# Kernel tuning notes

Hardware: AMD Instinct MI355X
Metric: run time of the kernel (lower is better)

## Reference

```python
import jax, jax.numpy as jnp
import numpy as np

B, S, H, NH, FF = 8, 512, 1024, 16, 4096
DK = H // NH


def _ln(x, g, b):
    m = x.mean(-1, keepdims=True)
    v = ((x - m) ** 2).mean(-1, keepdims=True)
    return (x - m) / jnp.sqrt(v + 1e-5) * g + b


def _fwd(x, predicate_pos, attn_bias, attention_mask, atom_graph, variable_graph,
         ln1_g, ln1_b, wq, bq, wk, bk, wv, bv, wo, bo,
         pq_w, pq_b, pk_w, pk_b, pv_w, pv_b, ln2_g, ln2_b, w1, b1, w2, b2):
    b_, s_, h_ = x.shape
    y = _ln(x, ln1_g, ln1_b)
    # ---- self attention (manual MHA with additive bias + mask) ----
    scale = DK ** -0.5
    q = (y @ wq + bq).reshape(b_, s_, NH, DK) * scale
    k = (y @ wk + bk).reshape(b_, s_, NH, DK)
    v = (y @ wv + bv).reshape(b_, s_, NH, DK)
    scores = jnp.einsum('bihd,bjhd->bhij', q, k)
    scores = scores + attn_bias[:, None, :, :] + attention_mask[:, None, :, :]
    att = jax.nn.softmax(scores, axis=-1)
    y_self = jnp.einsum('bhij,bjhd->bihd', att, v).reshape(b_, s_, h_) @ wo + bo
    # ---- path attention (single-head with graph biases) ----
    pscale = h_ ** -0.5
    pq = (y @ pq_w + pq_b) * pscale
    pk = y @ pk_w + pk_b
    pv = y @ pv_w + pv_b
    patt = jnp.einsum('bid,bjd->bij', pq, pk) + atom_graph + variable_graph
    patt = jax.nn.softmax(patt, axis=-1)
    xp = jnp.einsum('bij,bjd->bid', patt, pv)  # [B,S,H]
    # vectorized gather-mean over predicate positions (replaces per-sample loop)
    prev = jnp.concatenate([xp[:, :1], xp[:, :-1]], axis=1)   # xp[i-1]
    nxt = jnp.concatenate([xp[:, 1:], xp[:, -1:]], axis=1)    # xp[i+1]
    a0 = xp[:, 0:2].mean(axis=1, keepdims=True)               # i == 0
    a1 = xp[:, 0:3].mean(axis=1, keepdims=True)               # i == 1
    a2 = (xp + nxt) / 2.0                                     # pos[i-2] == 1
    a3 = (prev + xp + nxt) / 3.0                              # else
    i_arr = jnp.arange(s_)
    pos = (predicate_pos == 1)
    pos_m2 = jnp.pad(pos[:, :-2], ((0, 0), (2, 0)))           # pos[i-2], False for i<2
    atom = jnp.where(pos_m2[..., None], a2, a3)
    atom = jnp.where((i_arr == 1)[None, :, None], a1, atom)
    atom = jnp.where((i_arr == 0)[None, :, None], a0, atom)
    w = pos.astype(xp.dtype)
    path = (atom * w[..., None]).sum(1) / w.sum(1, keepdims=True)  # [B,H]
    y_path = jnp.broadcast_to(path[:, None, :], (b_, s_, h_))
    # ---- combine + residual + FFN ----
    x = x + (y_self + y_path) / 2.0
    y2 = _ln(x, ln2_g, ln2_b)
    hmid = jax.nn.gelu(y2 @ w1 + b1, approximate=False)
    return x + (hmid @ w2 + b2)


def setup_inputs() -> dict:
    key = jax.random.key(0)
    ks = jax.random.split(key, 16)
    def w(k, shape):
        return 0.02 * jax.random.normal(k, shape, dtype=jnp.float32)
    pp = jax.random.randint(ks[0], (B, S), 0, 2, dtype=jnp.int32)
    pp = pp.at[:, 2].set(1).at[:, -1].set(0)  # >=1 predicate; no predicate at last node
    return {
        'x': jax.random.normal(ks[1], (B, S, H), dtype=jnp.float32),
        'predicate_pos': pp,
        'variable_tags': jnp.zeros((B, S), dtype=jnp.int32),
        'attn_bias': 0.1 * jax.random.normal(ks[2], (B, S, S), dtype=jnp.float32),
        'attention_mask': jnp.zeros((B, S, S), dtype=jnp.float32),
        'atom_graph': 0.1 * jax.random.normal(ks[3], (B, S, S), dtype=jnp.float32),
        'variable_graph': 0.1 * jax.random.normal(ks[4], (B, S, S), dtype=jnp.float32),
        'ln1_g': jnp.ones((H,), jnp.float32), 'ln1_b': jnp.zeros((H,), jnp.float32),
        'wq': w(ks[5], (H, H)), 'bq': jnp.zeros((H,), jnp.float32),
        'wk': w(ks[6], (H, H)), 'bk': jnp.zeros((H,), jnp.float32),
        'wv': w(ks[7], (H, H)), 'bv': jnp.zeros((H,), jnp.float32),
        'wo': w(ks[8], (H, H)), 'bo': jnp.zeros((H,), jnp.float32),
        'pq_w': w(ks[9], (H, H)), 'pq_b': jnp.zeros((H,), jnp.float32),
        'pk_w': w(ks[10], (H, H)), 'pk_b': jnp.zeros((H,), jnp.float32),
        'pv_w': w(ks[11], (H, H)), 'pv_b': jnp.zeros((H,), jnp.float32),
        'ln2_g': jnp.ones((H,), jnp.float32), 'ln2_b': jnp.zeros((H,), jnp.float32),
        'w1': w(ks[12], (H, FF)), 'b1': jnp.zeros((FF,), jnp.float32),
        'w2': w(ks[13], (FF, H)), 'b2': jnp.zeros((H,), jnp.float32),
    }


def reference(x, predicate_pos, variable_tags, attn_bias, attention_mask, atom_graph, variable_graph,
              ln1_g, ln1_b, wq, bq, wk, bk, wv, bv, wo, bo,
              pq_w, pq_b, pk_w, pk_b, pv_w, pv_b, ln2_g, ln2_b, w1, b1, w2, b2):
    # variable_tags is unused in the original forward as well
    return _fwd(x, predicate_pos, attn_bias, attention_mask, atom_graph, variable_graph,
                ln1_g, ln1_b, wq, bq, wk, bk, wv, bv, wo, bo,
                pq_w, pq_b, pk_w, pk_b, pv_w, pv_b, ln2_g, ln2_b, w1, b1, w2, b2)
```

## Files before the change

kernel.cpp:

```cpp
#include <hip/hip_runtime.h>
#include <hip/hip_bf16.h>
#include <math.h>


typedef __bf16 bf16x8 __attribute__((ext_vector_type(8)));
typedef float f32x4 __attribute__((ext_vector_type(4)));

__device__ __forceinline__ void async_copy16(void* lds, const void* g) {
  __builtin_amdgcn_global_load_lds(
      (__attribute__((address_space(1))) void*)(void*)g,
      (__attribute__((address_space(3))) void*)lds, 16, 0, 0);
}

#define SB0 __builtin_amdgcn_sched_barrier(0)
#define BARRIER __builtin_amdgcn_s_barrier()

__global__ __launch_bounds__(256) void ln_rows_bf16(
    const float* __restrict__ X, const float* __restrict__ G,
    const float* __restrict__ Bt, __hip_bfloat16* __restrict__ O) {
  long row = blockIdx.x;
  int t = threadIdx.x;
  const float4 xv = ((const float4*)(X + row * 1024))[t];
  float s = xv.x + xv.y + xv.z + xv.w;
  float q = xv.x * xv.x + xv.y * xv.y + xv.z * xv.z + xv.w * xv.w;
#pragma unroll
  for (int o = 32; o; o >>= 1) {
    s += __shfl_xor(s, o);
    q += __shfl_xor(q, o);
  }
  __shared__ float rs[4], rq[4];
  int wid = t >> 6;
  if ((t & 63) == 0) { rs[wid] = s; rq[wid] = q; }
  __syncthreads();
  s = rs[0] + rs[1] + rs[2] + rs[3];
  q = rq[0] + rq[1] + rq[2] + rq[3];
  float mean = s * (1.f / 1024.f);
  float var = q * (1.f / 1024.f) - mean * mean;
  float rstd = rsqrtf(var + 1e-5f);
  const float4 gv = ((const float4*)G)[t];
  const float4 bv = ((const float4*)Bt)[t];
  __hip_bfloat16* o = O + row * 1024 + t * 4;
  o[0] = __float2bfloat16((xv.x - mean) * rstd * gv.x + bv.x);
  o[1] = __float2bfloat16((xv.y - mean) * rstd * gv.y + bv.y);
  o[2] = __float2bfloat16((xv.z - mean) * rstd * gv.z + bv.z);
  o[3] = __float2bfloat16((xv.w - mean) * rstd * gv.w + bv.w);
}

struct TC7 {
  const float* in[7];
  __hip_bfloat16* out[7];
  float scale[7];
};
__global__ __launch_bounds__(256) void tconv7(TC7 p) {
  __shared__ float t[32][33];
  int j = blockIdx.z;
  const float* in = p.in[j];
  __hip_bfloat16* out = p.out[j];
  float sc = p.scale[j];
  int c0 = blockIdx.x * 32, r0 = blockIdx.y * 32;
  int tid = threadIdx.x;
  int lr = tid >> 3, lc = (tid & 7) * 4;
  const float4 v = *(const float4*)&in[(long)(r0 + lr) * 1024 + c0 + lc];
  t[lr][lc] = v.x; t[lr][lc + 1] = v.y; t[lr][lc + 2] = v.z; t[lr][lc + 3] = v.w;
  __syncthreads();
  int oc = tid >> 3, orr = (tid & 7) * 4;
  __hip_bfloat16* o = &out[(long)(c0 + oc) * 1024 + r0 + orr];
  o[0] = __float2bfloat16(t[orr][oc] * sc);
  o[1] = __float2bfloat16(t[orr + 1][oc] * sc);
  o[2] = __float2bfloat16(t[orr + 2][oc] * sc);
  o[3] = __float2bfloat16(t[orr + 3][oc] * sc);
}

__global__ __launch_bounds__(256) void tconv_f32_bf16(
    const float* __restrict__ in, __hip_bfloat16* __restrict__ out, int R,
    int C) {
  __shared__ float t[32][33];
  int c0 = blockIdx.x * 32, r0 = blockIdx.y * 32;
  int tid = threadIdx.x;
  int lr = tid >> 3, lc = (tid & 7) * 4;
  const float4 v = *(const float4*)&in[(long)(r0 + lr) * C + c0 + lc];
  t[lr][lc] = v.x; t[lr][lc + 1] = v.y; t[lr][lc + 2] = v.z; t[lr][lc + 3] = v.w;
  __syncthreads();
  int oc = tid >> 3, orr = (tid & 7) * 4;
  __hip_bfloat16* o = &out[(long)(c0 + oc) * R + r0 + orr];
  o[0] = __float2bfloat16(t[orr][oc]);
  o[1] = __float2bfloat16(t[orr + 1][oc]);
  o[2] = __float2bfloat16(t[orr + 2][oc]);
  o[3] = __float2bfloat16(t[orr + 3][oc]);
}

__global__ __launch_bounds__(256) void tconv_bf16(
    const __hip_bfloat16* __restrict__ in, __hip_bfloat16* __restrict__ out,
    int R, int C, int ldin, long sIn) {
  __shared__ __hip_bfloat16 t[32][34];
  int bz = blockIdx.z;
  long ibase = (long)bz * sIn;
  long obase = (long)bz * R * C;
  int c0 = blockIdx.x * 32, r0 = blockIdx.y * 32;
  int tid = threadIdx.x;
  int lr = tid >> 3, lc = (tid & 7) * 4;
  const __hip_bfloat16* ip = &in[ibase + (long)(r0 + lr) * ldin + c0 + lc];
  t[lr][lc] = ip[0]; t[lr][lc + 1] = ip[1]; t[lr][lc + 2] = ip[2]; t[lr][lc + 3] = ip[3];
  __syncthreads();
  int oc = tid >> 3, orr = (tid & 7) * 4;
  __hip_bfloat16* o = &out[obase + (long)(c0 + oc) * R + r0 + orr];
  o[0] = t[orr][oc];
  o[1] = t[orr + 1][oc];
  o[2] = t[orr + 2][oc];
  o[3] = t[orr + 3][oc];
}

struct BC6 {
  const float* b[6];
  float scale[6];
};
__global__ __launch_bounds__(256) void bias_concat(BC6 p, float* __restrict__ o) {
  int idx = blockIdx.x * 256 + threadIdx.x;
  int j = idx >> 10, e = idx & 1023;
  o[idx] = p.b[j][e] * p.scale[j];
}

template <int BN>
__global__ __launch_bounds__(512, 2) void gemm256(
    const __hip_bfloat16* __restrict__ A, const __hip_bfloat16* __restrict__ Bt,
    const float* __restrict__ bias, void* __restrict__ C, int K, int lda,
    int ldb, int ldc, int act, int obf, long sC) {
  constexpr int NR = BN / 64;
  constexpr int ABYTES = 256 * 128;
  constexpr int BBYTES = BN * 128;
  constexpr int BUF = ABYTES + BBYTES;
  __shared__ char lds[2 * BUF];

  int bx, by;
  {
    int wg = blockIdx.y * gridDim.x + blockIdx.x;
    int gx = gridDim.x, gy = gridDim.y;
    if ((gx & 3) == 0 && (gy & 1) == 0) {
      int cw = gx >> 2, ch = gy >> 1;
      int xcd = wg & 7, idx = wg >> 3;
      bx = (xcd & 3) * cw + idx % cw;
      by = (xcd >> 2) * ch + idx / cw;
    } else {
      bx = blockIdx.x;
      by = blockIdx.y;
    }
  }
  const int m0 = by * 256, n0 = bx * BN;
  const int z = blockIdx.z;
  const long kbase = (long)z * K * 2;

  const int tid = threadIdx.x;
  const int lane = tid & 63, wid = tid >> 6;
  const int wm = wid >> 2, wn = wid & 3;
  const int ll = lane & 15, lh = lane >> 4;

  const char* Ag = (const char*)A;
  const char* Bg = (const char*)Bt;
  const int srow = tid >> 3;
  const int scb = (((tid & 7) ^ (srow & 7)) << 4);
  const int sld = (tid & 7) << 4;

  auto stageA = [&](char* base, long kb) {
#pragma unroll
    for (int l = 0; l < 4; ++l) {
      int row = l * 64 + srow;
      async_copy16(base + row * 128 + sld,
                   Ag + ((long)(m0 + row) * lda) * 2 + kb + scb);
    }
  };
  auto stageB = [&](char* base, long kb) {
#pragma unroll
    for (int l = 0; l < BN / 64; ++l) {
      int row = l * 64 + srow;
      async_copy16(base + ABYTES + row * 128 + sld,
                   Bg + ((long)(n0 + row) * ldb) * 2 + kb + scb);
    }
  };

  const int rx = ll & 7;
  const int ck[2] = {((0 + lh) ^ rx) << 4, ((4 + lh) ^ rx) << 4};

  f32x4 acc[8][NR];
#pragma unroll
  for (int m = 0; m < 8; ++m)
#pragma unroll
    for (int n = 0; n < NR; ++n) acc[m][n] = (f32x4){0.f, 0.f, 0.f, 0.f};

  const int nt = K >> 6;
  stageA(lds, kbase);
  stageB(lds, kbase);

  for (int t = 0; t < nt; ++t) {
    const int bt = t & 1;
    const char* Ab = lds + bt * BUF;
    const char* Bb = Ab + ABYTES;
    char* nb = lds + (bt ^ 1) * BUF;
    const bool pre = (t + 1 < nt);

    SB0; BARRIER; SB0;
    if (pre) {
      const long kb = kbase + (long)(t + 1) * 128;
      stageA(nb, kb);
      stageB(nb, kb);
      if constexpr (BN == 256)
        asm volatile("s_waitcnt vmcnt(8)" ::: "memory");
      else if constexpr (BN == 192)
        asm volatile("s_waitcnt vmcnt(7)" ::: "memory");
      else
        asm volatile("s_waitcnt vmcnt(6)" ::: "memory");
    } else {
      asm volatile("s_waitcnt vmcnt(0)" ::: "memory");
    }
    SB0; BARRIER; SB0;

#pragma unroll
    for (int ks = 0; ks < 2; ++ks) {
      bf16x8 bf[NR];
#pragma unroll
      for (int n = 0; n < NR; ++n)
        bf[n] = *(const bf16x8*)(Bb + (wn * (BN / 4) + n * 16 + ll) * 128 +
                                 ck[ks]);
      bf16x8 af[4];
#pragma unroll
      for (int m = 0; m < 4; ++m)
        af[m] = *(const bf16x8*)(Ab + (wm * 128 + m * 16 + ll) * 128 + ck[ks]);
      __builtin_amdgcn_s_setprio(1);
#pragma unroll
      for (int m = 0; m < 4; ++m)
#pragma unroll
        for (int n = 0; n < NR; ++n)
          acc[m][n] = __builtin_amdgcn_mfma_f32_16x16x32_bf16(af[m], bf[n],
                                                              acc[m][n], 0, 0, 0);
      __builtin_amdgcn_s_setprio(0);
#pragma unroll
      for (int m = 0; m < 4; ++m)
        af[m] = *(const bf16x8*)(Ab + (wm * 128 + (m + 4) * 16 + ll) * 128 +
                                 ck[ks]);
      __builtin_amdgcn_s_setprio(1);
#pragma unroll
      for (int m = 0; m < 4; ++m)
#pragma unroll
        for (int n = 0; n < NR; ++n)
          acc[m + 4][n] = __builtin_amdgcn_mfma_f32_16x16x32_bf16(
              af[m], bf[n], acc[m + 4][n], 0, 0, 0);
      __builtin_amdgcn_s_setprio(0);
    }
  }

#pragma unroll
  for (int m = 0; m < 8; ++m) {
    int row = m0 + wm * 128 + m * 16 + lh * 4;
#pragma unroll
    for (int n = 0; n < NR; ++n) {
      int col = n0 + wn * (BN / 4) + n * 16 + ll;
      float bs = bias ? bias[col] : 0.f;
#pragma unroll
      for (int r = 0; r < 4; ++r) {
        float v = acc[m][n][r] + bs;
        if (act) v = v * 0.5f * (1.f + erff(v * 0.70710678118f));
        long cidx = (long)z * sC + (long)(row + r) * ldc + col;
        if (obf)
          ((__hip_bfloat16*)C)[cidx] = __float2bfloat16(v);
        else
          ((float*)C)[cidx] = v;
      }
    }
  }
}

__global__ __launch_bounds__(256) void ffn2_reduce(
    const float* __restrict__ P, const float* __restrict__ X2,
    const float* __restrict__ b2, float* __restrict__ OUT) {
  int i = blockIdx.x * 256 + threadIdx.x;
  const long SP = 4194304;
  float4 a = ((const float4*)P)[i];
  float4 b = ((const float4*)(P + SP))[i];
  float4 c = ((const float4*)(P + 2 * SP))[i];
  float4 d = ((const float4*)(P + 3 * SP))[i];
  float4 xr = ((const float4*)X2)[i];
  const float4 bb = *(const float4*)(b2 + ((i & 255) * 4));
  float4 o;
  o.x = a.x + b.x + c.x + d.x + xr.x + bb.x;
  o.y = a.y + b.y + c.y + d.y + xr.y + bb.y;
  o.z = a.z + b.z + c.z + d.z + xr.z + bb.z;
  o.w = a.w + b.w + c.w + d.w + xr.w + bb.w;
  ((float4*)OUT)[i] = o;
}

__global__ __launch_bounds__(256) void gemm_bf16_nt(
    const __hip_bfloat16* __restrict__ A, const __hip_bfloat16* __restrict__ Bt,
    const float* __restrict__ bias, const float* __restrict__ E1,
    const float* __restrict__ E2, void* __restrict__ C, int K, int lda,
    int ldb, int ldc, long sA, long sB, long sC, long sE, float alpha, int act,
    int obf, int pbc) {
  __shared__ unsigned short AsU[128 * 32];
  __shared__ unsigned short BsU[128 * 32];
  const int tid = threadIdx.x;
  const int lane = tid & 63, wave = tid >> 6;
  const int wr = wave >> 1, wc = wave & 1;

  int nwg = gridDim.x * gridDim.y;
  int wg = blockIdx.y * gridDim.x + blockIdx.x;
  int bx = blockIdx.x, by = blockIdx.y;
  if ((nwg & 7) == 0) {
    int cpx = nwg >> 3;
    int sw = (wg & 7) * cpx + (wg >> 3);
    bx = sw % gridDim.x;
    by = sw / gridDim.x;
  }
  const int m0 = by * 128, n0 = bx * 128;
  const int bz = blockIdx.z;
  const char* Ab = (const char*)(A + (long)bz * sA);
  const char* Bb = (const char*)(Bt + (long)bz * sB);

  f32x4 acc[4][4];
#pragma unroll
  for (int m = 0; m < 4; ++m)
#pragma unroll
    for (int n = 0; n < 4; ++n) acc[m][n] = (f32x4){0.f, 0.f, 0.f, 0.f};

  const int srow = tid >> 2;
  const int scol = (tid & 3) * 16;
  const int wbase = (tid >> 6) * 1024;

  for (int k0 = 0; k0 < K; k0 += 32) {
#pragma unroll
    for (int i = 0; i < 2; ++i) {
      async_copy16((char*)AsU + i * 4096 + wbase,
                   Ab + ((long)(m0 + i * 64 + srow) * lda + k0) * 2 + scol);
      async_copy16((char*)BsU + i * 4096 + wbase,
                   Bb + ((long)(n0 + i * 64 + srow) * ldb + k0) * 2 + scol);
    }
    __syncthreads();

    const int koff = (lane >> 4) * 8;
    bf16x8 a[4], b[4];
#pragma unroll
    for (int m = 0; m < 4; ++m)
      a[m] = *(const bf16x8*)&AsU[(wr * 64 + m * 16 + (lane & 15)) * 32 + koff];
#pragma unroll
    for (int n = 0; n < 4; ++n)
      b[n] = *(const bf16x8*)&BsU[(wc * 64 + n * 16 + (lane & 15)) * 32 + koff];
#pragma unroll
    for (int m = 0; m < 4; ++m)
#pragma unroll
      for (int n = 0; n < 4; ++n)
        acc[m][n] = __builtin_amdgcn_mfma_f32_16x16x32_bf16(a[m], b[n],
                                                            acc[m][n], 0, 0, 0);
    __syncthreads();
  }

#pragma unroll
  for (int m = 0; m < 4; ++m) {
    int row = m0 + wr * 64 + m * 16 + (lane >> 4) * 4;
#pragma unroll
    for (int n = 0; n < 4; ++n) {
      int col = n0 + wc * 64 + n * 16 + (lane & 15);
      float bs = bias ? bias[col] : 0.f;
#pragma unroll
      for (int r = 0; r < 4; ++r) {
        float v = (acc[m][n][r] + bs) * alpha;
        if (pbc) {
          v = E1[(long)(row + r) * ldc + col] +
              0.5f * (v + E2[(long)((row + r) >> 9) * 1024 + col]);
        } else {
          long eidx = (long)bz * sE + (long)(row + r) * ldc + col;
          if (E1) v += E1[eidx];
          if (E2) v += E2[eidx];
        }
        if (act) v = v * 0.5f * (1.f + erff(v * 0.70710678118f));
        long cidx = (long)bz * sC + (long)(row + r) * ldc + col;
        if (obf)
          ((__hip_bfloat16*)C)[cidx] = __float2bfloat16(v);
        else
          ((float*)C)[cidx] = v;
      }
    }
  }
}

__global__ __launch_bounds__(256) void attn_mfma(
    const __hip_bfloat16* __restrict__ Q, const __hip_bfloat16* __restrict__ K,
    const __hip_bfloat16* __restrict__ VT, const float* __restrict__ BiasP,
    const float* __restrict__ MaskP, __hip_bfloat16* __restrict__ O,
    int ldqk) {
  __shared__ __hip_bfloat16 P[32][520];
  __shared__ float red[2][32][4];
  const int it = blockIdx.x, h = blockIdx.y, b = blockIdx.z;
  const int i0 = it * 32;
  const int tid = threadIdx.x;
  const int lane = tid & 63, w = tid >> 6;
  const int lh = lane >> 4, ll = lane & 15;

  const long qkb = (long)b * 512 * ldqk + h * 64;

  bf16x8 a[2][2];
#pragma unroll
  for (int m = 0; m < 2; ++m)
#pragma unroll
    for (int ks = 0; ks < 2; ++ks)
      a[m][ks] = *(const bf16x8*)&Q[qkb + (long)(i0 + m * 16 + ll) * ldqk +
                                    ks * 32 + lh * 8];

  f32x4 acc[2][8];
#pragma unroll
  for (int m = 0; m < 2; ++m)
#pragma unroll
    for (int n = 0; n < 8; ++n) acc[m][n] = (f32x4){0.f, 0.f, 0.f, 0.f};

#pragma unroll
  for (int n = 0; n < 8; ++n) {
    const __hip_bfloat16* kp =
        &K[qkb + (long)(w * 128 + n * 16 + ll) * ldqk + lh * 8];
    bf16x8 b0 = *(const bf16x8*)&kp[0];
    bf16x8 b1 = *(const bf16x8*)&kp[32];
#pragma unroll
    for (int m = 0; m < 2; ++m) {
      acc[m][n] =
          __builtin_amdgcn_mfma_f32_16x16x32_bf16(a[m][0], b0, acc[m][n], 0, 0, 0);
      acc[m][n] =
          __builtin_amdgcn_mfma_f32_16x16x32_bf16(a[m][1], b1, acc[m][n], 0, 0, 0);
    }
  }

  const long bmo = ((long)b * 512 + i0) * 512 + w * 128;
#pragma unroll
  for (int m = 0; m < 2; ++m)
#pragma unroll
    for (int r = 0; r < 4; ++r) {
      int row = m * 16 + lh * 4 + r;
#pragma unroll
      for (int n = 0; n < 8; ++n) {
        long gi = bmo + (long)row * 512 + n * 16 + ll;
        acc[m][n][r] += BiasP[gi] + MaskP[gi];
      }
    }

  float rmax[2][4];
#pragma unroll
  for (int m = 0; m < 2; ++m)
#pragma unroll
    for (int r = 0; r < 4; ++r) {
      float v = acc[m][0][r];
#pragma unroll
      for (int n = 1; n < 8; ++n) v = fmaxf(v, acc[m][n][r]);
#pragma unroll
      for (int o = 1; o < 16; o <<= 1) v = fmaxf(v, __shfl_xor(v, o));
      rmax[m][r] = v;
    }
  if (ll == 0) {
#pragma unroll
    for (int m = 0; m < 2; ++m)
#pragma unroll
      for (int r = 0; r < 4; ++r) red[0][m * 16 + lh * 4 + r][w] = rmax[m][r];
  }
  __syncthreads();
#pragma unroll
  for (int m = 0; m < 2; ++m)
#pragma unroll
    for (int r = 0; r < 4; ++r) {
      const float* p = red[0][m * 16 + lh * 4 + r];
      rmax[m][r] = fmaxf(fmaxf(p[0], p[1]), fmaxf(p[2], p[3]));
    }
  float rsum[2][4];
#pragma unroll
  for (int m = 0; m < 2; ++m)
#pragma unroll
    for (int r = 0; r < 4; ++r) {
      float s = 0.f;
#pragma unroll
      for (int n = 0; n < 8; ++n) {
        float e = __expf(acc[m][n][r] - rmax[m][r]);
        acc[m][n][r] = e;
        s += e;
      }
#pragma unroll
      for (int o = 1; o < 16; o <<= 1) s += __shfl_xor(s, o);
      rsum[m][r] = s;
    }
  if (ll == 0) {
#pragma unroll
    for (int m = 0; m < 2; ++m)
#pragma unroll
      for (int r = 0; r < 4; ++r) red[1][m * 16 + lh * 4 + r][w] = rsum[m][r];
  }
  __syncthreads();
#pragma unroll
  for (int m = 0; m < 2; ++m)
#pragma unroll
    for (int r = 0; r < 4; ++r) {
      const float* p = red[1][m * 16 + lh * 4 + r];
      float inv = 1.f / (p[0] + p[1] + p[2] + p[3]);
      int row = m * 16 + lh * 4 + r;
#pragma unroll
      for (int n = 0; n < 8; ++n)
        P[row][w * 128 + n * 16 + ll] = __float2bfloat16(acc[m][n][r] * inv);
    }
  __syncthreads();

  const long vtb = ((long)b * 1024 + h * 64) * 512;
  const long ob = (long)b * 512 * 1024 + h * 64;
  const int mw = (w >> 1) * 16, nw = (w & 1) * 32;
  f32x4 oacc[2];
  oacc[0] = (f32x4){0.f, 0.f, 0.f, 0.f};
  oacc[1] = (f32x4){0.f, 0.f, 0.f, 0.f};
#pragma unroll
  for (int ks = 0; ks < 16; ++ks) {
    int k0 = ks * 32;
    bf16x8 pa = *(const bf16x8*)&P[mw + ll][k0 + lh * 8];
#pragma unroll
    for (int nf = 0; nf < 2; ++nf) {
      bf16x8 vb = *(const bf16x8*)&VT[vtb + (long)(nw + nf * 16 + ll) * 512 +
                                      k0 + lh * 8];
      oacc[nf] =
          __builtin_amdgcn_mfma_f32_16x16x32_bf16(pa, vb, oacc[nf], 0, 0, 0);
    }
  }
#pragma unroll
  for (int nf = 0; nf < 2; ++nf)
#pragma unroll
    for (int r = 0; r < 4; ++r)
      O[ob + (long)(i0 + mw + lh * 4 + r) * 1024 + nw + nf * 16 + ll] =
          __float2bfloat16(oacc[nf][r]);
}

__global__ __launch_bounds__(256) void softmax_rows(
    const float* __restrict__ P, __hip_bfloat16* __restrict__ Ob) {
  const float* row = P + (long)blockIdx.x * 512;
  __hip_bfloat16* orow = Ob + (long)blockIdx.x * 512;
  int t = threadIdx.x;
  float v0 = row[t], v1 = row[t + 256];
  float m = fmaxf(v0, v1);
#pragma unroll
  for (int o = 32; o; o >>= 1) m = fmaxf(m, __shfl_xor(m, o));
  __shared__ float red[8];
  int wid = t >> 6, lane = t & 63;
  if (!lane) red[wid] = m;
  __syncthreads();
  m = fmaxf(fmaxf(red[0], red[1]), fmaxf(red[2], red[3]));
  float e0 = __expf(v0 - m), e1 = __expf(v1 - m);
  float s = e0 + e1;
#pragma unroll
  for (int o = 32; o; o >>= 1) s += __shfl_xor(s, o);
  if (!lane) red[4 + wid] = s;
  __syncthreads();
  s = red[4] + red[5] + red[6] + red[7];
  float inv = 1.f / s;
  orow[t] = __float2bfloat16(e0 * inv);
  orow[t + 256] = __float2bfloat16(e1 * inv);
}

__global__ __launch_bounds__(256) void path_partial(
    const float* __restrict__ xp, const int* __restrict__ pp,
    float* __restrict__ PP, float* __restrict__ WS) {
  int b = blockIdx.x, hc = blockIdx.y, ic = blockIdx.z;
  int h = hc * 256 + threadIdx.x;
  const int* ppb = pp + b * 512;
  const float* xb = xp + (long)b * 512 * 1024;
  int iA = ic * 64, iB = iA + 64;
  float acc = 0.f;
  for (int i = iA; i < iB; ++i) {
    if (ppb[i] != 1) continue;
    float cur = xb[(long)i * 1024 + h];
    float a;
    if (i == 0) {
      a = 0.5f * (cur + xb[1024 + h]);
    } else if (i == 1) {
      a = (xb[h] + cur + xb[2 * 1024 + h]) * (1.f / 3.f);
    } else {
      int inx = (i + 1 < 512) ? i + 1 : 511;
      float nx = xb[(long)inx * 1024 + h];
      if (ppb[i - 2] == 1) {
        a = 0.5f * (cur + nx);
      } else {
        a = (xb[(long)(i - 1) * 1024 + h] + cur + nx) * (1.f / 3.f);
      }
    }
    acc += a;
  }
  PP[((long)b * 8 + ic) * 1024 + h] = acc;
  if (hc == 0 && threadIdx.x == 0) {
    float c = 0.f;
    for (int i = iA; i < iB; ++i) c += (ppb[i] == 1) ? 1.f : 0.f;
    WS[b * 8 + ic] = c;
  }
}

__global__ __launch_bounds__(256) void path_finalize(
    const float* __restrict__ PP, const float* __restrict__ WS,
    float* __restrict__ PATH) {
  int b = blockIdx.x;
  int h = blockIdx.y * 256 + threadIdx.x;
  float s = 0.f, w = 0.f;
#pragma unroll
  for (int ic = 0; ic < 8; ++ic) {
    s += PP[((long)b * 8 + ic) * 1024 + h];
    w += WS[b * 8 + ic];
  }
  PATH[b * 1024 + h] = s / w;
}

extern "C" void kernel_launch(void* const* d_in, const int* in_sizes, int n_in,
                              void* d_out, int out_size, void* d_ws,
                              size_t ws_size, hipStream_t stream) {
  const float* x = (const float*)d_in[0];
  const int* pp = (const int*)d_in[1];
  const float* abias = (const float*)d_in[3];
  const float* amask = (const float*)d_in[4];
  const float* agraph = (const float*)d_in[5];
  const float* vgraph = (const float*)d_in[6];
  const float* ln1g = (const float*)d_in[7];
  const float* ln1b = (const float*)d_in[8];
  const float* wq = (const float*)d_in[9];
  const float* bq = (const float*)d_in[10];
  const float* wk = (const float*)d_in[11];
  const float* bk = (const float*)d_in[12];
  const float* wv = (const float*)d_in[13];
  const float* bv = (const float*)d_in[14];
  const float* wo = (const float*)d_in[15];
  const float* bo = (const float*)d_in[16];
  const float* pqw = (const float*)d_in[17];
  const float* pqb = (const float*)d_in[18];
  const float* pkw = (const float*)d_in[19];
  const float* pkb = (const float*)d_in[20];
  const float* pvw = (const float*)d_in[21];
  const float* pvb = (const float*)d_in[22];
  const float* ln2g = (const float*)d_in[23];
  const float* ln2b = (const float*)d_in[24];
  const float* w1 = (const float*)d_in[25];
  const float* b1 = (const float*)d_in[26];
  const float* w2 = (const float*)d_in[27];
  const float* b2 = (const float*)d_in[28];

  char* wsb = (char*)d_ws;
  auto Ybf = (__hip_bfloat16*)(wsb);
  auto QKV = (__hip_bfloat16*)(wsb + (8l << 20));
  auto VTb = (__hip_bfloat16*)(wsb + (56l << 20));
  auto PVT = (__hip_bfloat16*)(wsb + (64l << 20));
  auto ATTb = (__hip_bfloat16*)(wsb + (72l << 20));
  auto PATTb = (__hip_bfloat16*)(wsb + (88l << 20));
  auto PATTf = (float*)(wsb + (92l << 20));
  auto XP = (float*)(wsb + (92l << 20));
  auto WALL = (__hip_bfloat16*)(wsb + (108l << 20));
  auto WOT = (__hip_bfloat16*)(wsb + (120l << 20));
  auto W1T = (__hip_bfloat16*)(wsb + (122l << 20));
  auto bias6 = (float*)(wsb + (130l << 20));
  auto PPart = (float*)(wsb + (131l << 20));
  auto WSp = (float*)(wsb + (132l << 20));
  auto PATH = (float*)(wsb + (133l << 20));
  auto X2 = (float*)(wsb + (24l << 20));
  auto HMID = (__hip_bfloat16*)(wsb + (40l << 20));
  auto W2T = ATTb;
  auto PART = (float*)(wsb + (92l << 20));
  __hip_bfloat16* Y2b = Ybf;
  float* OUT = (float*)d_out;

  const float qscale = 0.125f;
  const float pscale = 0.03125f;
  const long S2 = 512l * 512;
  const long SQ = 512l * 6144;

  __hip_bfloat16* Qp = QKV;
  __hip_bfloat16* Kp = QKV + 1024;
  __hip_bfloat16* Vp = QKV + 2048;
  __hip_bfloat16* PQp = QKV + 3072;
  __hip_bfloat16* PKp = QKV + 4096;
  __hip_bfloat16* PVp = QKV + 5120;

  TC7 tp;
  tp.in[0] = wq;  tp.out[0] = WALL;                 tp.scale[0] = qscale;
  tp.in[1] = wk;  tp.out[1] = WALL + 1024 * 1024;   tp.scale[1] = 1.f;
  tp.in[2] = wv;  tp.out[2] = WALL + 2048 * 1024;   tp.scale[2] = 1.f;
  tp.in[3] = pqw; tp.out[3] = WALL + 3072 * 1024;   tp.scale[3] = pscale;
  tp.in[4] = pkw; tp.out[4] = WALL + 4096 * 1024;   tp.scale[4] = 1.f;
  tp.in[5] = pvw; tp.out[5] = WALL + 5120 * 1024;   tp.scale[5] = 1.f;
  tp.in[6] = wo;  tp.out[6] = WOT;                  tp.scale[6] = 1.f;
  tconv7<<<dim3(32, 32, 7), 256, 0, stream>>>(tp);
  tconv_f32_bf16<<<dim3(128, 32), 256, 0, stream>>>(w1, W1T, 1024, 4096);

  BC6 bp;
  bp.b[0] = bq;  bp.scale[0] = qscale;
  bp.b[1] = bk;  bp.scale[1] = 1.f;
  bp.b[2] = bv;  bp.scale[2] = 1.f;
  bp.b[3] = pqb; bp.scale[3] = pscale;
  bp.b[4] = pkb; bp.scale[4] = 1.f;
  bp.b[5] = pvb; bp.scale[5] = 1.f;
  bias_concat<<<24, 256, 0, stream>>>(bp, bias6);

  ln_rows_bf16<<<4096, 256, 0, stream>>>(x, ln1g, ln1b, Ybf);

  gemm256<192><<<dim3(32, 16, 1), 512, 0, stream>>>(
      Ybf, WALL, bias6, QKV, 1024, 1024, 1024, 6144, 0, 1, 0);

  tconv_bf16<<<dim3(32, 16, 8), 256, 0, stream>>>(Vp, VTb, 512, 1024, 6144, SQ);
  tconv_bf16<<<dim3(32, 16, 8), 256, 0, stream>>>(PVp, PVT, 512, 1024, 6144, SQ);

  gemm_bf16_nt<<<dim3(4, 4, 8), 256, 0, stream>>>(
      PQp, PKp, nullptr, agraph, vgraph, PATTf, 1024, 6144, 6144, 512, SQ, SQ,
      S2, S2, 1.f, 0, 0, 0);
  softmax_rows<<<4096, 256, 0, stream>>>(PATTf, PATTb);

  attn_mfma<<<dim3(16, 16, 8), 256, 0, stream>>>(Qp, Kp, VTb, abias, amask,
                                                 ATTb, 6144);

  gemm_bf16_nt<<<dim3(8, 4, 8), 256, 0, stream>>>(
      PATTb, PVT, nullptr, nullptr, nullptr, XP, 512, 512, 512, 1024, S2,
      512l * 1024, 512l * 1024, 0, 1.f, 0, 0, 0);

  path_partial<<<dim3(8, 4, 8), 256, 0, stream>>>(XP, pp, PPart, WSp);
  path_finalize<<<dim3(8, 4), 256, 0, stream>>>(PPart, WSp, PATH);

  gemm_bf16_nt<<<dim3(8, 32, 1), 256, 0, stream>>>(
      ATTb, WOT, bo, x, PATH, X2, 1024, 1024, 1024, 1024, 0, 0, 0, 0, 1.f, 0,
      0, 1);

  tconv_f32_bf16<<<dim3(32, 128), 256, 0, stream>>>(w2, W2T, 4096, 1024);

  ln_rows_bf16<<<4096, 256, 0, stream>>>(X2, ln2g, ln2b, Y2b);

  gemm256<256><<<dim3(16, 16, 1), 512, 0, stream>>>(
      Y2b, W1T, b1, HMID, 1024, 1024, 1024, 4096, 1, 1, 0);

  gemm256<256><<<dim3(4, 16, 4), 512, 0, stream>>>(
      HMID, W2T, nullptr, PART, 1024, 4096, 4096, 1024, 0, 0, 4194304);

  ffn2_reduce<<<4096, 256, 0, stream>>>(PART, X2, b2, OUT);
}
```

Baseline: 470.4 us.

## Double-buffer LDS in NT GEMM and split-K the path score GEMM

The generic NT GEMM now keeps two LDS buffers. It issues async global-to-LDS copies for the next K tile while MFMAs run on the current one, and raises wave priority around the MFMA block. It also gains a K-split parameter. The path-attention score GEMM uses it with two splits to double the block count on an undersubscribed grid, and the softmax kernel sums the two fp32 partials before normalising. The costs are double the LDS footprint, which may reduce occupancy, an extra 8 MB partial buffer in the workspace that must not overlap other data, and extra read traffic in the softmax.

```diff
diff --git a/kernel.cpp b/kernel.cpp
--- a/kernel.cpp
+++ b/kernel.cpp
@@ -292,9 +292,9 @@
     const float* __restrict__ bias, const float* __restrict__ E1,
     const float* __restrict__ E2, void* __restrict__ C, int K, int lda,
     int ldb, int ldc, long sA, long sB, long sC, long sE, float alpha, int act,
-    int obf, int pbc) {
-  __shared__ unsigned short AsU[128 * 32];
-  __shared__ unsigned short BsU[128 * 32];
+    int obf, int pbc, int ksplit, long sSplit) {
+  __shared__ unsigned short AsU[2][128 * 32];
+  __shared__ unsigned short BsU[2][128 * 32];
   const int tid = threadIdx.x;
   const int lane = tid & 63, wave = tid >> 6;
   const int wr = wave >> 1, wc = wave & 1;
@@ -309,7 +309,10 @@
     by = sw / gridDim.x;
   }
   const int m0 = by * 128, n0 = bx * 128;
-  const int bz = blockIdx.z;
+  const int bz = blockIdx.z / ksplit;
+  const int sk = blockIdx.z % ksplit;
+  if (sk != 0) { bias = nullptr; E1 = nullptr; E2 = nullptr; }
+  const int kcol0 = sk * K;
   const char* Ab = (const char*)(A + (long)bz * sA);
   const char* Bb = (const char*)(Bt + (long)bz * sB);
 
@@ -323,31 +326,49 @@
   const int scol = (tid & 3) * 16;
   const int wbase = (tid >> 6) * 1024;
 
-  for (int k0 = 0; k0 < K; k0 += 32) {
+  auto stage = [&](int buf, int k0) {
+    int kk = kcol0 + k0;
 #pragma unroll
     for (int i = 0; i < 2; ++i) {
-      async_copy16((char*)AsU + i * 4096 + wbase,
-                   Ab + ((long)(m0 + i * 64 + srow) * lda + k0) * 2 + scol);
-      async_copy16((char*)BsU + i * 4096 + wbase,
-                   Bb + ((long)(n0 + i * 64 + srow) * ldb + k0) * 2 + scol);
-    }
-    __syncthreads();
+      async_copy16((char*)AsU[buf] + i * 4096 + wbase,
+                   Ab + ((long)(m0 + i * 64 + srow) * lda + kk) * 2 + scol);
+      async_copy16((char*)BsU[buf] + i * 4096 + wbase,
+                   Bb + ((long)(n0 + i * 64 + srow) * ldb + kk) * 2 + scol);
+    }
+  };
+
+  const int ntk = K >> 5;
+  stage(0, 0);
+
+  for (int t = 0; t < ntk; ++t) {
+    const int bt = t & 1;
+    SB0; BARRIER; SB0;
+    if (t + 1 < ntk) {
+      stage(bt ^ 1, (t + 1) * 32);
+      asm volatile("s_waitcnt vmcnt(4)" ::: "memory");
+    } else {
+      asm volatile("s_waitcnt vmcnt(0)" ::: "memory");
+    }
+    SB0; BARRIER; SB0;
 
     const int koff = (lane >> 4) * 8;
     bf16x8 a[4], b[4];
 #pragma unroll
     for (int m = 0; m < 4; ++m)
-      a[m] = *(const bf16x8*)&AsU[(wr * 64 + m * 16 + (lane & 15)) * 32 + koff];
+      a[m] = *(const bf16x8*)&AsU[bt][(wr * 64 + m * 16 + (lane & 15)) * 32 +
+                                      koff];
 #pragma unroll
     for (int n = 0; n < 4; ++n)
-      b[n] = *(const bf16x8*)&BsU[(wc * 64 + n * 16 + (lane & 15)) * 32 + koff];
+      b[n] = *(const bf16x8*)&BsU[bt][(wc * 64 + n * 16 + (lane & 15)) * 32 +
+                                      koff];
+    __builtin_amdgcn_s_setprio(1);
 #pragma unroll
     for (int m = 0; m < 4; ++m)
 #pragma unroll
       for (int n = 0; n < 4; ++n)
         acc[m][n] = __builtin_amdgcn_mfma_f32_16x16x32_bf16(a[m], b[n],
                                                             acc[m][n], 0, 0, 0);
-    __syncthreads();
+    __builtin_amdgcn_s_setprio(0);
   }
 
 #pragma unroll
@@ -369,7 +390,8 @@
           if (E2) v += E2[eidx];
         }
         if (act) v = v * 0.5f * (1.f + erff(v * 0.70710678118f));
-        long cidx = (long)bz * sC + (long)(row + r) * ldc + col;
+        long cidx = (long)bz * sC + (long)sk * sSplit +
+                    (long)(row + r) * ldc + col;
         if (obf)
           ((__hip_bfloat16*)C)[cidx] = __float2bfloat16(v);
         else
@@ -524,12 +546,14 @@
           __float2bfloat16(oacc[nf][r]);
 }
 
-__global__ __launch_bounds__(256) void softmax_rows(
-    const float* __restrict__ P, __hip_bfloat16* __restrict__ Ob) {
-  const float* row = P + (long)blockIdx.x * 512;
+__global__ __launch_bounds__(256) void softmax_rows2(
+    const float* __restrict__ P0, const float* __restrict__ P1,
+    __hip_bfloat16* __restrict__ Ob) {
+  const float* r0 = P0 + (long)blockIdx.x * 512;
+  const float* r1 = P1 + (long)blockIdx.x * 512;
   __hip_bfloat16* orow = Ob + (long)blockIdx.x * 512;
   int t = threadIdx.x;
-  float v0 = row[t], v1 = row[t + 256];
+  float v0 = r0[t] + r1[t], v1 = r0[t + 256] + r1[t + 256];
   float m = fmaxf(v0, v1);
 #pragma unroll
   for (int o = 32; o; o >>= 1) m = fmaxf(m, __shfl_xor(m, o));
@@ -659,6 +683,7 @@
   const float pscale = 0.03125f;
   const long S2 = 512l * 512;
   const long SQ = 512l * 6144;
+  const long SPLT = 8l * S2;
 
   __hip_bfloat16* Qp = QKV;
   __hip_bfloat16* Kp = QKV + 1024;
@@ -695,24 +720,24 @@
   tconv_bf16<<<dim3(32, 16, 8), 256, 0, stream>>>(Vp, VTb, 512, 1024, 6144, SQ);
   tconv_bf16<<<dim3(32, 16, 8), 256, 0, stream>>>(PVp, PVT, 512, 1024, 6144, SQ);
 
-  gemm_bf16_nt<<<dim3(4, 4, 8), 256, 0, stream>>>(
-      PQp, PKp, nullptr, agraph, vgraph, PATTf, 1024, 6144, 6144, 512, SQ, SQ,
-      S2, S2, 1.f, 0, 0, 0);
-  softmax_rows<<<4096, 256, 0, stream>>>(PATTf, PATTb);
+  gemm_bf16_nt<<<dim3(4, 4, 16), 256, 0, stream>>>(
+      PQp, PKp, nullptr, agraph, vgraph, PATTf, 512, 6144, 6144, 512, SQ, SQ,
+      S2, S2, 1.f, 0, 0, 0, 2, SPLT);
+  softmax_rows2<<<4096, 256, 0, stream>>>(PATTf, PATTf + SPLT, PATTb);
 
   attn_mfma<<<dim3(16, 16, 8), 256, 0, stream>>>(Qp, Kp, VTb, abias, amask,
                                                  ATTb, 6144);
 
   gemm_bf16_nt<<<dim3(8, 4, 8), 256, 0, stream>>>(
       PATTb, PVT, nullptr, nullptr, nullptr, XP, 512, 512, 512, 1024, S2,
-      512l * 1024, 512l * 1024, 0, 1.f, 0, 0, 0);
+      512l * 1024, 512l * 1024, 0, 1.f, 0, 0, 0, 1, 0);
 
   path_partial<<<dim3(8, 4, 8), 256, 0, stream>>>(XP, pp, PPart, WSp);
   path_finalize<<<dim3(8, 4), 256, 0, stream>>>(PPart, WSp, PATH);
 
   gemm_bf16_nt<<<dim3(8, 32, 1), 256, 0, stream>>>(
       ATTb, WOT, bo, x, PATH, X2, 1024, 1024, 1024, 1024, 0, 0, 0, 0, 1.f, 0,
-      0, 1);
+      0, 1, 1, 0);
 
   tconv_f32_bf16<<<dim3(32, 128), 256, 0, stream>>>(w2, W2T, 4096, 1024);
 
```

Result: faster. 452.4 us (-3.8%).
